# Kernel optimization log

Hardware: AMD Instinct MI355X
Metric: run time of the kernel (lower is better)

## Reference

```python
import jax, jax.numpy as jnp
import numpy as np

EPS_CB = 1e-6   # ConvBlock norm_layer eps
EPS_LVC = 1e-5  # default BatchNorm2d/1d eps in LVC branch


def _conv(x, w, stride=1, pad=0):
    return jax.lax.conv_general_dilated(
        x, w, (stride, stride), [(pad, pad), (pad, pad)],
        dimension_numbers=("NCHW", "OIHW", "NCHW"))


def _bn2d(x, g, b, eps):
    # inference-style BN with running_mean=0, running_var=1
    inv = 1.0 / jnp.sqrt(1.0 + eps)
    return x * (g * inv)[None, :, None, None] + b[None, :, None, None]


def setup_inputs() -> dict:
    key = jax.random.key(0)
    ks = jax.random.split(key, 24)
    B, C, Cm, K, H, W = 32, 512, 128, 64, 32, 32
    rn = lambda k, s, sc=0.05: jax.random.normal(k, s, dtype=jnp.float32) * sc
    std = 1.0 / (K * C) ** 0.5
    return {
        "x": jax.random.normal(ks[0], (B, C, H, W), dtype=jnp.float32),
        "c1_w": rn(ks[1], (Cm, C, 1, 1)),
        "bn1_g": 1.0 + rn(ks[2], (Cm,)), "bn1_b": rn(ks[3], (Cm,)),
        "c2_w": rn(ks[4], (Cm, Cm, 3, 3)),
        "bn2_g": 1.0 + rn(ks[5], (Cm,)), "bn2_b": rn(ks[6], (Cm,)),
        "c3_w": rn(ks[7], (C, Cm, 1, 1)),
        "bn3_g": 1.0 + rn(ks[8], (C,)), "bn3_b": rn(ks[9], (C,)),
        "rc_w": rn(ks[10], (C, C, 1, 1)),
        "rbn_g": 1.0 + rn(ks[11], (C,)), "rbn_b": rn(ks[12], (C,)),
        "lvc_w": rn(ks[13], (C, C, 1, 1)),
        "lvcbn_g": 1.0 + rn(ks[14], (C,)), "lvcbn_b": rn(ks[15], (C,)),
        "codewords": jax.random.uniform(ks[16], (K, C), minval=-std, maxval=std, dtype=jnp.float32),
        "scale": jax.random.uniform(ks[17], (K,), minval=-1.0, maxval=0.0, dtype=jnp.float32),
        "enbn_g": 1.0 + rn(ks[18], (K,)), "enbn_b": rn(ks[19], (K,)),
        "fc_w": rn(ks[20], (C, C)), "fc_b": rn(ks[21], (C,)),
    }


def reference(x, c1_w, bn1_g, bn1_b, c2_w, bn2_g, bn2_b, c3_w, bn3_g, bn3_b,
              rc_w, rbn_g, rbn_b, lvc_w, lvcbn_g, lvcbn_b,
              codewords, scale, enbn_g, enbn_b, fc_w, fc_b):
    # ---- ConvBlock (ResNet bottleneck with residual 1x1 conv) ----
    h = jax.nn.relu(_bn2d(_conv(x, c1_w), bn1_g, bn1_b, EPS_CB))
    h = jax.nn.relu(_bn2d(_conv(h, c2_w, pad=1), bn2_g, bn2_b, EPS_CB))
    h = _bn2d(_conv(h, c3_w), bn3_g, bn3_b, EPS_CB)
    r = _bn2d(_conv(x, rc_w), rbn_g, rbn_b, EPS_CB)
    xb = jax.nn.relu(h + r)  # (B,C,H,W)

    # ---- LVC: 1x1 conv + BN + ReLU, then Encoding ----
    e = jax.nn.relu(_bn2d(_conv(xb, lvc_w), lvcbn_g, lvcbn_b, EPS_LVC))
    B, C, H, W = e.shape
    ef = e.reshape(B, C, H * W).transpose(0, 2, 1)  # (B,N,C)

    x2 = jnp.sum(ef * ef, axis=-1)                       # (B,N)
    c2 = jnp.sum(codewords * codewords, axis=-1)         # (K,)
    xc = jnp.einsum("bnc,kc->bnk", ef, codewords)        # (B,N,K)
    sl2 = scale[None, None, :] * (x2[:, :, None] - 2.0 * xc + c2[None, None, :])
    a = jax.nn.softmax(sl2, axis=2)                      # (B,N,K)

    # aggregate: sum_n a_{nk} (x_n - c_k)
    enc = jnp.einsum("bnk,bnc->bkc", a, ef) \
          - jnp.sum(a, axis=1)[:, :, None] * codewords[None, :, :]  # (B,K,C)

    # BatchNorm1d over the K (channel) axis, inference-style, then ReLU
    inv = 1.0 / jnp.sqrt(1.0 + EPS_LVC)
    enc = jax.nn.relu(enc * (enbn_g * inv)[None, :, None] + enbn_b[None, :, None])
    en = jnp.mean(enc, axis=1)                           # (B,C)

    # ---- SE-style gating ----
    gam = jax.nn.sigmoid(en @ fc_w.T + fc_b)             # (B,C)
    return jax.nn.relu(xb + xb * gam[:, :, None, None])
```

## Files before the change

kernel.cpp:

```cpp
#include <hip/hip_runtime.h>
#include <math.h>

constexpr int BATCH = 32;
constexpr int C     = 512;
constexpr int CM    = 128;
constexpr int KW    = 64;
constexpr int NPIX  = 1024;

typedef unsigned short u16;
typedef __attribute__((ext_vector_type(8))) short bf16x8;
typedef __attribute__((ext_vector_type(4))) float f32x4;
typedef __attribute__((ext_vector_type(4))) unsigned short u16x4;
typedef __attribute__((ext_vector_type(8))) unsigned short u16x8;

__device__ __forceinline__ float bf2f(u16 u) {
    unsigned int v = ((unsigned int)u) << 16;
    return __uint_as_float(v);
}
__device__ __forceinline__ u16 f2bf(float f) {
    unsigned int u = __float_as_uint(f);
    u = u + 0x7FFFu + ((u >> 16) & 1u);
    return (u16)(u >> 16);
}
__device__ __forceinline__ float4 ld4(const float* p) {
    return *reinterpret_cast<const float4*>(p);
}
__device__ __forceinline__ void gload16(const u16* g, u16* l) {
    __builtin_amdgcn_global_load_lds((const __attribute__((address_space(1))) void*)g,
                                     (__attribute__((address_space(3))) void*)l, 16, 0, 0);
}

template<int MODE, int TM, bool RELU, bool WTR>
__global__ __launch_bounds__(256)
void gemm_mfma(const u16* __restrict__ A1, const u16* __restrict__ A2,
               const u16* __restrict__ Wm, u16* __restrict__ outB,
               u16* __restrict__ outT,
               const float* __restrict__ scale, const float* __restrict__ bias,
               const u16* __restrict__ zbuf, int K, int Cout)
{
    constexpr int MF = TM / 32;
    __shared__ __align__(16) u16 As[2][TM * 32];
    __shared__ __align__(16) u16 Bs[2][4096];
    const int b   = blockIdx.z;
    const int n0  = blockIdx.x * TM;
    const int co0 = blockIdx.y * 128;
    const int t    = threadIdx.x;
    const int lane = t & 63;
    const int w    = t >> 6;
    const int wr = w >> 1, wc = w & 1;
    const int lhi = lane >> 4, llo = lane & 15;

    f32x4 acc[MF][4];
#pragma unroll
    for (int i = 0; i < MF; ++i)
#pragma unroll
        for (int j = 0; j < 4; ++j) acc[i][j] = (f32x4){0.f, 0.f, 0.f, 0.f};

    const int aBase = lhi * TM + wr * (TM / 2) + llo;
    const int bBase = lhi * 128 + wc * 64 + llo;
    const int nt = K / 32;

    auto stage = [&](int buf, int k0) {
#pragma unroll
        for (int rd = 0; rd < (TM * 4) / 256; ++rd) {
            int ch = t + rd * 256;
            int g  = ch / TM, r = ch % TM;
            int kg = k0 + g * 8;
            const u16* src;
            if (MODE == 0) {
                src = A1 + ((size_t)((b << 10) + n0 + r)) * (size_t)K + kg;
            } else if (MODE == 1) {
                int tap = kg >> 7, ci = kg & 127;
                int n = n0 + r;
                int y = (n >> 5) + tap / 3 - 1;
                int x = (n & 31) + tap % 3 - 1;
                src = ((unsigned)y < 32u && (unsigned)x < 32u)
                    ? A1 + ((size_t)((b << 10) + y * 32 + x)) * 128 + ci
                    : zbuf;
            } else {
                src = (kg < 128)
                    ? A1 + ((size_t)((b << 10) + n0 + r)) * 128 + kg
                    : A2 + ((size_t)((b << 10) + n0 + r)) * 512 + (kg - 128);
            }
            gload16(src, &As[buf][ch * 8]);
        }
#pragma unroll
        for (int rd = 0; rd < 2; ++rd) {
            int ch = t + rd * 256;
            int g = ch >> 7, r = ch & 127;
            gload16(Wm + (size_t)(co0 + r) * (size_t)K + k0 + g * 8, &Bs[buf][ch * 8]);
        }
    };

    stage(0, 0);
    __syncthreads();
    int cur = 0;
    for (int ti = 0; ti < nt; ++ti) {
        if (ti + 1 < nt) stage(cur ^ 1, (ti + 1) * 32);
        const bf16x8* Av = (const bf16x8*)As[cur];
        const bf16x8* Bv = (const bf16x8*)Bs[cur];
        bf16x8 af[MF], bfr[4];
#pragma unroll
        for (int m = 0; m < MF; ++m)  af[m]  = Av[aBase + m * 16];
#pragma unroll
        for (int nf = 0; nf < 4; ++nf) bfr[nf] = Bv[bBase + nf * 16];
#pragma unroll
        for (int m = 0; m < MF; ++m)
#pragma unroll
            for (int nf = 0; nf < 4; ++nf)
                acc[m][nf] = __builtin_amdgcn_mfma_f32_16x16x32_bf16(af[m], bfr[nf], acc[m][nf], 0, 0, 0);
        __syncthreads();
        cur ^= 1;
    }
#pragma unroll
    for (int nf = 0; nf < 4; ++nf) {
        int coL = co0 + wc * 64 + nf * 16 + llo;
        float s  = scale ? scale[coL] : 1.f;
        float bi = bias  ? bias[coL]  : 0.f;
#pragma unroll
        for (int m = 0; m < MF; ++m) {
            f32x4 v = acc[m][nf];
            int rowb = n0 + wr * (TM / 2) + m * 16 + lhi * 4;
            u16 o[4];
#pragma unroll
            for (int q = 0; q < 4; ++q) {
                float val = fmaf(v[q], s, bi);
                if (RELU) val = fmaxf(val, 0.f);
                o[q] = f2bf(val);
                outB[((size_t)((b << 10) + rowb + q)) * (size_t)Cout + coL] = o[q];
            }
            if (WTR) {
                u16x4 ov;
                ov[0] = o[0]; ov[1] = o[1]; ov[2] = o[2]; ov[3] = o[3];
                *(u16x4*)(outT + (((size_t)(b * Cout + coL)) << 10) + rowb) = ov;
            }
        }
    }
}

__global__ __launch_bounds__(256)
void gemm_xc(const u16* __restrict__ e, const u16* __restrict__ cwb,
             const float* __restrict__ scale, const float* __restrict__ c2,
             u16* __restrict__ a_t, float* __restrict__ asum)
{
    const int b  = blockIdx.y;
    const int n0 = blockIdx.x * 64;
    const int t    = threadIdx.x;
    const int lane = t & 63;
    const int w    = t >> 6;
    const int wr = w >> 1, wc = w & 1;
    const int lhi = lane >> 4, llo = lane & 15;

    __shared__ __align__(16) char smem[16640];
    u16* As = (u16*)smem;
    u16* Bs = (u16*)(smem + 4096);
    float (*sm)[65] = (float(*)[65])smem;
    __shared__ float x2s[64], pmax[64][4], psum[64][4], sc_s[64], c2_s[64];
    if (t < 64) { sc_s[t] = scale[t]; c2_s[t] = c2[t]; }

    f32x4 acc[2][2];
#pragma unroll
    for (int i = 0; i < 2; ++i)
#pragma unroll
        for (int j = 0; j < 2; ++j) acc[i][j] = (f32x4){0.f, 0.f, 0.f, 0.f};
    float x2p = 0.f;
    const int aBase = lhi * 64 + wr * 32 + llo;
    const int bBase = lhi * 64 + wc * 32 + llo;
    const int xr = w * 16 + (lane >> 2);
    const int xg = lane & 3;

    const int g = t >> 6, r = t & 63;
    for (int k0 = 0; k0 < 512; k0 += 32) {
        gload16(e + ((size_t)((b << 10) + n0 + r)) * 512 + k0 + g * 8, &As[t * 8]);
        gload16(cwb + (size_t)r * 512 + k0 + g * 8, &Bs[t * 8]);
        __syncthreads();
        {
            u16x8 vv = *(const u16x8*)&As[(xg * 64 + xr) * 8];
#pragma unroll
            for (int j = 0; j < 8; ++j) { float f = bf2f(vv[j]); x2p = fmaf(f, f, x2p); }
        }
        const bf16x8* Av = (const bf16x8*)As;
        const bf16x8* Bv = (const bf16x8*)Bs;
        bf16x8 af[2], bfr[2];
#pragma unroll
        for (int m = 0; m < 2; ++m)  af[m]  = Av[aBase + m * 16];
#pragma unroll
        for (int nf = 0; nf < 2; ++nf) bfr[nf] = Bv[bBase + nf * 16];
#pragma unroll
        for (int m = 0; m < 2; ++m)
#pragma unroll
            for (int nf = 0; nf < 2; ++nf)
                acc[m][nf] = __builtin_amdgcn_mfma_f32_16x16x32_bf16(af[m], bfr[nf], acc[m][nf], 0, 0, 0);
        __syncthreads();
    }
    float xs = x2p + __shfl_xor(x2p, 1, 64);
    xs += __shfl_xor(xs, 2, 64);
    if ((lane & 3) == 0) x2s[xr] = xs;
    __syncthreads();
#pragma unroll
    for (int m = 0; m < 2; ++m)
#pragma unroll
        for (int nf = 0; nf < 2; ++nf)
#pragma unroll
            for (int q = 0; q < 4; ++q) {
                int rr = wr * 32 + m * 16 + lhi * 4 + q;
                int cc = wc * 32 + nf * 16 + llo;
                sm[rr][cc] = sc_s[cc] * (x2s[rr] - 2.f * acc[m][nf][q] + c2_s[cc]);
            }
    __syncthreads();
    const int gq = t >> 6;
    float vloc[16];
    float pm = -1e30f;
#pragma unroll
    for (int j = 0; j < 16; ++j) { float v = sm[r][gq * 16 + j]; vloc[j] = v; pm = fmaxf(pm, v); }
    pmax[r][gq] = pm;
    __syncthreads();
    float mm = fmaxf(fmaxf(pmax[r][0], pmax[r][1]), fmaxf(pmax[r][2], pmax[r][3]));
    float ps = 0.f;
#pragma unroll
    for (int j = 0; j < 16; ++j) { float p = __expf(vloc[j] - mm); vloc[j] = p; ps += p; }
    psum[r][gq] = ps;
    __syncthreads();
    float inv = 1.f / (psum[r][0] + psum[r][1] + psum[r][2] + psum[r][3]);
#pragma unroll
    for (int j = 0; j < 16; ++j) {
        int k = gq * 16 + j;
        float av = vloc[j] * inv;
        a_t[((size_t)((b << 6) + k) << 10) + n0 + r] = f2bf(av);
        sm[r][k] = av;
    }
    __syncthreads();
    const int kk = t & 63, rg = t >> 6;
    float pa = 0.f;
#pragma unroll
    for (int j = 0; j < 16; ++j) pa += sm[rg * 16 + j][kk];
    atomicAdd(&asum[(b << 6) + kk], pa);
}

__global__ __launch_bounds__(256)
void enc_mfma(const u16* __restrict__ a_t, const u16* __restrict__ e_t,
              const float* __restrict__ cw, const float* __restrict__ asum,
              const float* __restrict__ sK, const float* __restrict__ bK,
              float* __restrict__ en)
{
    const int b  = blockIdx.y;
    const int c0 = blockIdx.x * 64;
    const int t    = threadIdx.x;
    const int lane = t & 63;
    const int w    = t >> 6;
    const int lhi = lane >> 4, llo = lane & 15;
    __shared__ __align__(16) u16 As[2048];
    __shared__ __align__(16) u16 Bs[2048];
    f32x4 acc[4];
#pragma unroll
    for (int i = 0; i < 4; ++i) acc[i] = (f32x4){0.f, 0.f, 0.f, 0.f};
    const int aBase = lhi * 64 + llo;
    const int bBase = lhi * 64 + w * 16 + llo;
    const int g = t >> 6, r = t & 63;

    for (int n0 = 0; n0 < NPIX; n0 += 32) {
        gload16(a_t + ((size_t)((b << 6) + r) << 10) + n0 + g * 8, &As[t * 8]);
        gload16(e_t + ((size_t)((b << 9) + c0 + r) << 10) + n0 + g * 8, &Bs[t * 8]);
        __syncthreads();
        const bf16x8* Av = (const bf16x8*)As;
        const bf16x8* Bv = (const bf16x8*)Bs;
        bf16x8 bfr = Bv[bBase];
#pragma unroll
        for (int m = 0; m < 4; ++m)
            acc[m] = __builtin_amdgcn_mfma_f32_16x16x32_bf16(Av[aBase + m * 16], bfr, acc[m], 0, 0, 0);
        __syncthreads();
    }
    const int c = c0 + w * 16 + llo;
    float s = 0.f;
#pragma unroll
    for (int m = 0; m < 4; ++m)
#pragma unroll
        for (int q = 0; q < 4; ++q) {
            int k = m * 16 + lhi * 4 + q;
            float v = acc[m][q] - asum[(b << 6) + k] * cw[((size_t)k << 9) + c];
            v = fmaxf(fmaf(v, sK[k], bK[k]), 0.f);
            s += v;
        }
    s += __shfl_xor(s, 16, 64);
    s += __shfl_xor(s, 32, 64);
    if (lane < 16) en[(size_t)(b << 9) + c] = s * (1.f / 64.f);
}

__global__ __launch_bounds__(256)
void tr_in_k(const float* __restrict__ x, u16* __restrict__ xbf)
{
    __shared__ float tile[64][65];
    int b = blockIdx.z, n0 = blockIdx.x * 64, c0 = blockIdx.y * 64, t = threadIdx.x;
#pragma unroll
    for (int q = 0; q < 16; ++q) {
        int idx = t + 256 * q;
        int c = idx >> 6, n = idx & 63;
        tile[c][n] = x[((size_t)((b << 9) + c0 + c) << 10) + n0 + n];
    }
    __syncthreads();
#pragma unroll
    for (int q = 0; q < 16; ++q) {
        int idx = t + 256 * q;
        int nn = idx >> 6, cc = idx & 63;
        xbf[((size_t)((b << 10) + n0 + nn) << 9) + c0 + cc] = f2bf(tile[cc][nn]);
    }
}

__global__ __launch_bounds__(256)
void final_tr_k(const u16* __restrict__ xb, const float* __restrict__ gam,
                float* __restrict__ out)
{
    __shared__ float tile[64][65];
    int b = blockIdx.z, n0 = blockIdx.x * 64, c0 = blockIdx.y * 64, t = threadIdx.x;
#pragma unroll
    for (int q = 0; q < 16; ++q) {
        int idx = t + 256 * q;
        int n = idx >> 6, c = idx & 63;
        float gm = 1.f + gam[(b << 9) + c0 + c];
        float v = bf2f(xb[((size_t)((b << 10) + n0 + n) << 9) + c0 + c]) * gm;
        tile[n][c] = fmaxf(v, 0.f);
    }
    __syncthreads();
#pragma unroll
    for (int q = 0; q < 16; ++q) {
        int idx = t + 256 * q;
        int cc = idx >> 6, nn = idx & 63;
        out[((size_t)((b << 9) + c0 + cc) << 10) + n0 + nn] = tile[nn][cc];
    }
}

__global__ __launch_bounds__(256)
void gam_k(const float* __restrict__ en, const float* __restrict__ fcw,
           const float* __restrict__ fcb, float* __restrict__ gam)
{
    int b = blockIdx.x;
    int c = blockIdx.y * 256 + threadIdx.x;
    __shared__ float es[C];
    es[threadIdx.x]       = en[(size_t)b * C + threadIdx.x];
    es[threadIdx.x + 256] = en[(size_t)b * C + threadIdx.x + 256];
    __syncthreads();
    float s = fcb[c];
    const float* wp = fcw + (size_t)c * C;
    for (int i = 0; i < C; i += 4) {
        float4 wv = ld4(wp + i);
        s = fmaf(es[i], wv.x, s);
        s = fmaf(es[i + 1], wv.y, s);
        s = fmaf(es[i + 2], wv.z, s);
        s = fmaf(es[i + 3], wv.w, s);
    }
    gam[(size_t)b * C + c] = 1.f / (1.f + __expf(-s));
}

__global__ __launch_bounds__(256)
void prep_all_k(const float* c1w, const float* bn1g, const float* bn2g,
                const float* c2w, const float* c3w, const float* bn3g,
                const float* bn3b, const float* rcw, const float* rbng,
                const float* rbnb, const float* lvcw, const float* lvcbng,
                const float* enbng, const float* cw,
                u16* c1b, u16* w2b, u16* wcatb, u16* lvcb, u16* cwb,
                float* s1, float* s2, float* slvc, float* bcat,
                float* sK, float* c2, float* asum, u16* zbuf)
{
    const float invCB  = rsqrtf(1.f + 1e-6f);
    const float invLVC = rsqrtf(1.f + 1e-5f);
    long id = (long)blockIdx.x * 256 + threadIdx.x;
    if (id < 327680) {
        int co = (int)(id / 640), k = (int)(id % 640);
        float v = (k < 128) ? c3w[co * 128 + k] * (bn3g[co] * invCB)
                            : rcw[co * 512 + (k - 128)] * (rbng[co] * invCB);
        wcatb[id] = f2bf(v);
        return;
    }
    id -= 327680;
    if (id < 147456) {
        int co = (int)(id / 1152), k = (int)(id % 1152);
        int tap = k >> 7, ci = k & 127;
        w2b[id] = f2bf(c2w[co * 1152 + ci * 9 + tap]);
        return;
    }
    id -= 147456;
    if (id < 262144) { lvcb[id] = f2bf(lvcw[id]); return; }
    id -= 262144;
    if (id < 65536)  { c1b[id]  = f2bf(c1w[id]);  return; }
    id -= 65536;
    if (id < 32768)  { cwb[id]  = f2bf(cw[id]);   return; }
    id -= 32768;
    if (id < 2048)   { asum[id] = 0.f; return; }
    id -= 2048;
    if (id < 1024)   { zbuf[id] = 0;   return; }
    id -= 1024;
    if (id < 128) { s1[id] = bn1g[id] * invCB; return; }
    id -= 128;
    if (id < 128) { s2[id] = bn2g[id] * invCB; return; }
    id -= 128;
    if (id < 512) { slvc[id] = lvcbng[id] * invLVC; return; }
    id -= 512;
    if (id < 512) { bcat[id] = bn3b[id] + rbnb[id]; return; }
    id -= 512;
    if (id < 64)  { sK[id] = enbng[id] * invLVC; return; }
    id -= 64;
    if (id < 64) {
        float s = 0.f;
        for (int c = 0; c < C; ++c) s = fmaf(cw[id * C + c], cw[id * C + c], s);
        c2[id] = s;
    }
}

extern "C" void kernel_launch(void* const* d_in, const int* in_sizes, int n_in,
                              void* d_out, int out_size, void* d_ws, size_t ws_size,
                              hipStream_t stream)
{
    const float* x      = (const float*)d_in[0];
    const float* c1w    = (const float*)d_in[1];
    const float* bn1g   = (const float*)d_in[2];
    const float* bn1b   = (const float*)d_in[3];
    const float* c2w    = (const float*)d_in[4];
    const float* bn2g   = (const float*)d_in[5];
    const float* bn2b   = (const float*)d_in[6];
    const float* c3w    = (const float*)d_in[7];
    const float* bn3g   = (const float*)d_in[8];
    const float* bn3b   = (const float*)d_in[9];
    const float* rcw    = (const float*)d_in[10];
    const float* rbng   = (const float*)d_in[11];
    const float* rbnb   = (const float*)d_in[12];
    const float* lvcw   = (const float*)d_in[13];
    const float* lvcbng = (const float*)d_in[14];
    const float* lvcbnb = (const float*)d_in[15];
    const float* cw     = (const float*)d_in[16];
    const float* scale  = (const float*)d_in[17];
    const float* enbng  = (const float*)d_in[18];
    const float* enbnb  = (const float*)d_in[19];
    const float* fcw    = (const float*)d_in[20];
    const float* fcb    = (const float*)d_in[21];
    float* out = (float*)d_out;
    char* W = (char*)d_ws;

    u16*  xbf  = (u16*)(W);
    u16*  e_b  = xbf;
    u16*  h1   = (u16*)(W + 33554432);
    u16*  a_t  = h1;
    u16*  h2   = (u16*)(W + 41943040);
    u16*  xb_b = (u16*)(W + 50331648);
    u16*  e_t  = (u16*)(W + 83886080);
    char* wb   = W + 117440512;
    u16* c1b   = (u16*)(wb);
    u16* w2b   = (u16*)(wb + 131072);
    u16* wcatb = (u16*)(wb + 425984);
    u16* lvcb  = (u16*)(wb + 1081344);
    u16* cwb   = (u16*)(wb + 1605632);
    float* fb  = (float*)(wb + 1671168);
    float* asum = fb;
    float* en   = fb + 2048;
    float* gam  = fb + 18432;
    float* s1   = fb + 34816;
    float* s2   = s1 + 128;
    float* slvc = s2 + 128;
    float* bcat = slvc + 512;
    float* sK   = bcat + 512;
    float* c2   = sK + 64;
    u16* zbuf   = (u16*)(c2 + 64);

    prep_all_k<<<3282, 256, 0, stream>>>(c1w, bn1g, bn2g, c2w, c3w, bn3g, bn3b,
                                         rcw, rbng, rbnb, lvcw, lvcbng, enbng, cw,
                                         c1b, w2b, wcatb, lvcb, cwb,
                                         s1, s2, slvc, bcat, sK, c2, asum, zbuf);

    tr_in_k<<<dim3(16, 8, 32), 256, 0, stream>>>(x, xbf);

    gemm_mfma<0, 64, true, false><<<dim3(16, 1, 32), 256, 0, stream>>>(
        xbf, nullptr, c1b, h1, nullptr, s1, bn1b, zbuf, 512, 128);
    gemm_mfma<1, 64, true, false><<<dim3(16, 1, 32), 256, 0, stream>>>(
        h1, nullptr, w2b, h2, nullptr, s2, bn2b, zbuf, 1152, 128);
    gemm_mfma<2, 128, true, false><<<dim3(8, 4, 32), 256, 0, stream>>>(
        h2, xbf, wcatb, xb_b, nullptr, nullptr, bcat, zbuf, 640, 512);
    gemm_mfma<0, 128, true, true><<<dim3(8, 4, 32), 256, 0, stream>>>(
        xb_b, nullptr, lvcb, e_b, e_t, slvc, lvcbnb, zbuf, 512, 512);
    gemm_xc<<<dim3(16, 32), 256, 0, stream>>>(e_b, cwb, scale, c2, a_t, asum);
    enc_mfma<<<dim3(8, 32), 256, 0, stream>>>(a_t, e_t, cw, asum, sK, enbnb, en);
    gam_k<<<dim3(32, 2), 256, 0, stream>>>(en, fcw, fcb, gam);
    final_tr_k<<<dim3(16, 8, 32), 256, 0, stream>>>(xb_b, gam, out);
}
```

Baseline: 385.2 us.

## Replace double-buffered K=32 GEMM staging with single-buffer K=64 tiles

The MFMA GEMM kernel drops double buffering. Each iteration now loads a K-chunk of 64 into a single LDS buffer, syncs, and runs two MFMA sub-steps per load. This halves the number of barriers and loop iterations. In exchange, global-to-LDS loads no longer overlap with MFMA compute, which exposes memory latency unless occupancy hides it.

```diff
diff --git a/kernel.cpp b/kernel.cpp
--- a/kernel.cpp
+++ b/kernel.cpp
@@ -39,8 +39,8 @@
                const u16* __restrict__ zbuf, int K, int Cout)
 {
     constexpr int MF = TM / 32;
-    __shared__ __align__(16) u16 As[2][TM * 32];
-    __shared__ __align__(16) u16 Bs[2][4096];
+    __shared__ __align__(16) u16 As[TM * 64];
+    __shared__ __align__(16) u16 Bs[128 * 64];
     const int b   = blockIdx.z;
     const int n0  = blockIdx.x * TM;
     const int co0 = blockIdx.y * 128;
@@ -56,13 +56,9 @@
 #pragma unroll
         for (int j = 0; j < 4; ++j) acc[i][j] = (f32x4){0.f, 0.f, 0.f, 0.f};
 
-    const int aBase = lhi * TM + wr * (TM / 2) + llo;
-    const int bBase = lhi * 128 + wc * 64 + llo;
-    const int nt = K / 32;
-
-    auto stage = [&](int buf, int k0) {
-#pragma unroll
-        for (int rd = 0; rd < (TM * 4) / 256; ++rd) {
+    for (int k0 = 0; k0 < K; k0 += 64) {
+#pragma unroll
+        for (int rd = 0; rd < (TM * 8) / 256; ++rd) {
             int ch = t + rd * 256;
             int g  = ch / TM, r = ch % TM;
             int kg = k0 + g * 8;
@@ -82,35 +78,33 @@
                     ? A1 + ((size_t)((b << 10) + n0 + r)) * 128 + kg
                     : A2 + ((size_t)((b << 10) + n0 + r)) * 512 + (kg - 128);
             }
-            gload16(src, &As[buf][ch * 8]);
-        }
-#pragma unroll
-        for (int rd = 0; rd < 2; ++rd) {
+            gload16(src, &As[ch * 8]);
+        }
+#pragma unroll
+        for (int rd = 0; rd < 4; ++rd) {
             int ch = t + rd * 256;
             int g = ch >> 7, r = ch & 127;
-            gload16(Wm + (size_t)(co0 + r) * (size_t)K + k0 + g * 8, &Bs[buf][ch * 8]);
-        }
-    };
-
-    stage(0, 0);
-    __syncthreads();
-    int cur = 0;
-    for (int ti = 0; ti < nt; ++ti) {
-        if (ti + 1 < nt) stage(cur ^ 1, (ti + 1) * 32);
-        const bf16x8* Av = (const bf16x8*)As[cur];
-        const bf16x8* Bv = (const bf16x8*)Bs[cur];
-        bf16x8 af[MF], bfr[4];
-#pragma unroll
-        for (int m = 0; m < MF; ++m)  af[m]  = Av[aBase + m * 16];
-#pragma unroll
-        for (int nf = 0; nf < 4; ++nf) bfr[nf] = Bv[bBase + nf * 16];
-#pragma unroll
-        for (int m = 0; m < MF; ++m)
+            gload16(Wm + (size_t)(co0 + r) * (size_t)K + k0 + g * 8, &Bs[ch * 8]);
+        }
+        __syncthreads();
+        const bf16x8* Av = (const bf16x8*)As;
+        const bf16x8* Bv = (const bf16x8*)Bs;
+#pragma unroll
+        for (int kk = 0; kk < 2; ++kk) {
+            bf16x8 af[MF], bfr[4];
+#pragma unroll
+            for (int m = 0; m < MF; ++m)
+                af[m] = Av[(kk * 4 + lhi) * TM + wr * (TM / 2) + m * 16 + llo];
 #pragma unroll
             for (int nf = 0; nf < 4; ++nf)
-                acc[m][nf] = __builtin_amdgcn_mfma_f32_16x16x32_bf16(af[m], bfr[nf], acc[m][nf], 0, 0, 0);
-        __syncthreads();
-        cur ^= 1;
+                bfr[nf] = Bv[(kk * 4 + lhi) * 128 + wc * 64 + nf * 16 + llo];
+#pragma unroll
+            for (int m = 0; m < MF; ++m)
+#pragma unroll
+                for (int nf = 0; nf < 4; ++nf)
+                    acc[m][nf] = __builtin_amdgcn_mfma_f32_16x16x32_bf16(af[m], bfr[nf], acc[m][nf], 0, 0, 0);
+        }
+        __syncthreads();
     }
 #pragma unroll
     for (int nf = 0; nf < 4; ++nf) {
```

New measurement: 384.4 us. About the same (-0.2%).
